# Kernel optimization log

Measured on AMD Instinct MI355X. Metric: run time of the kernel, lower is better.

The kernel has to match this reference:

```python
import jax, jax.numpy as jnp
import numpy as np


def _fps_indices(xyz, num_points):
    """Furthest point sampling. xyz: [B, N, 3] -> indices [B, num_points] (int32)."""
    B, N, _ = xyz.shape

    def step(carry, _):
        dist, farthest = carry                                   # dist: [B, N], farthest: [B]
        centroid = jnp.take_along_axis(xyz, farthest[:, None, None], axis=1)  # [B, 1, 3]
        d = jnp.sum((xyz - centroid) ** 2, axis=-1)              # [B, N]
        dist = jnp.minimum(dist, d)
        nxt = jnp.argmax(dist, axis=-1).astype(jnp.int32)        # [B]
        return (dist, nxt), farthest

    init = (jnp.full((B, N), jnp.inf, dtype=xyz.dtype),
            jnp.zeros((B,), dtype=jnp.int32))                    # convention: start at index 0
    _, idxs = jax.lax.scan(step, init, None, length=num_points)  # [num_points, B]
    return idxs.T                                                # [B, num_points]


def setup_inputs() -> dict:
    key = jax.random.key(0)
    B, C, N = 16, 3, 131072
    points = jax.random.normal(key, (B, C, N), dtype=jnp.float32)
    return {"points": points, "num_points": 2048}


def reference(points, num_points):
    # points: [B, 3, N] channels-first, as in the torch module
    xyz = jnp.transpose(points, (0, 2, 1))                       # [B, N, 3]
    idx = _fps_indices(xyz, num_points)                          # [B, num_points]
    # fps_gather_by_index: gather along the point dim of the channels-first tensor
    new_points = jnp.take_along_axis(points, idx[:, None, :], axis=2)  # [B, 3, num_points]
    return new_points
```

## Files before the change

kernel.cpp:

```cpp
#include <hip/hip_runtime.h>
#include <stdint.h>


#define NBATCH    16
#define NPTS      131072
#define SUBBLOCKS 16
#define NTHREADS  1024
#define CHUNK     8192
#define HALF      4096

typedef unsigned long long u64;

__device__ __forceinline__ u64 umax64(u64 a, u64 b) { return a > b ? a : b; }

__global__ __launch_bounds__(NTHREADS, 4)
void fps_kernel(const float* __restrict__ points,
                float* __restrict__ out,
                u64* __restrict__ slots, int M)
{
  __shared__ u64 wkeys[NTHREADS / 64];
  __shared__ u64 winner_s;

  const int bid   = blockIdx.x;
  const int xcd   = bid & 7;
  const int ord   = bid >> 3;
  const int batch = xcd * 2 + (ord >> 4);
  const int sub   = ord & 15;
  const int tid   = threadIdx.x;
  const int wave  = tid >> 6;
  const int lane  = tid & 63;

  const float* __restrict__ px = points + (size_t)batch * 3 * NPTS;
  const float* __restrict__ py = px + NPTS;
  const float* __restrict__ pz = px + 2 * NPTS;
  float* outb = out + (size_t)batch * 3 * M;
  u64* bslots = slots + (size_t)batch * 2 * SUBBLOCKS;

  const int cbase = sub * CHUNK;
  const int g0 = cbase + (tid << 2);
  const int g1 = g0 + HALF;

  float4 A0 = *(const float4*)(px + g0);
  float4 B0 = *(const float4*)(py + g0);
  float4 C0 = *(const float4*)(pz + g0);
  float4 A1 = *(const float4*)(px + g1);
  float4 B1 = *(const float4*)(py + g1);
  float4 C1 = *(const float4*)(pz + g1);
  float x0=A0.x, x1=A0.y, x2=A0.z, x3=A0.w, x4=A1.x, x5=A1.y, x6=A1.z, x7=A1.w;
  float y0=B0.x, y1=B0.y, y2=B0.z, y3=B0.w, y4=B1.x, y5=B1.y, y6=B1.z, y7=B1.w;
  float z0=C0.x, z1=C0.y, z2=C0.z, z3=C0.w, z4=C1.x, z5=C1.y, z6=C1.z, z7=C1.w;
  asm volatile("" :
    "+v"(x0),"+v"(x1),"+v"(x2),"+v"(x3),"+v"(x4),"+v"(x5),"+v"(x6),"+v"(x7),
    "+v"(y0),"+v"(y1),"+v"(y2),"+v"(y3),"+v"(y4),"+v"(y5),"+v"(y6),"+v"(y7),
    "+v"(z0),"+v"(z1),"+v"(z2),"+v"(z3),"+v"(z4),"+v"(z5),"+v"(z6),"+v"(z7));

  float d0, d1, d2, d3, d4, d5, d6, d7;
  d0 = d1 = d2 = d3 = d4 = d5 = d6 = d7 = __builtin_inff();

  if (sub == 0 && tid == 0) {
    outb[0]     = px[0];
    outb[M]     = py[0];
    outb[2 * M] = pz[0];
  }

  int sel = 0;
  for (int t = 1; t < M; ++t) {
    float cx = px[sel], cy = py[sel], cz = pz[sel];

    float best = -1.0f;
    int bidx = 0;
#define STEP(XX, YY, ZZ, DREG, IDX) { \
    float dx = __fsub_rn((XX), cx); \
    float dy = __fsub_rn((YY), cy); \
    float dz = __fsub_rn((ZZ), cz); \
    float dd = __builtin_fmaf(dz, dz, __builtin_fmaf(dy, dy, __fmul_rn(dx, dx))); \
    DREG = DREG < dd ? DREG : dd; \
    if (DREG > best) { best = DREG; bidx = (IDX); } }
    STEP(x0, y0, z0, d0, g0 + 0)
    STEP(x1, y1, z1, d1, g0 + 1)
    STEP(x2, y2, z2, d2, g0 + 2)
    STEP(x3, y3, z3, d3, g0 + 3)
    STEP(x4, y4, z4, d4, g1 + 0)
    STEP(x5, y5, z5, d5, g1 + 1)
    STEP(x6, y6, z6, d6, g1 + 2)
    STEP(x7, y7, z7, d7, g1 + 3)

    u64 key = ((u64)__float_as_uint(best) << 17) | (u64)((NPTS - 1) - bidx);

#pragma unroll
    for (int m = 32; m >= 1; m >>= 1) {
      u64 o = __shfl_xor(key, m, 64);
      key = umax64(key, o);
    }
    if (lane == 0) wkeys[wave] = key;
    __syncthreads();

    if (wave == 0) {
      u64 k = wkeys[lane & 15];
#pragma unroll
      for (int m = 8; m >= 1; m >>= 1) {
        u64 o = __shfl_xor(k, m, 64);
        k = umax64(k, o);
      }
      u64* par = bslots + (size_t)(t & 1) * SUBBLOCKS;

      if (lane == 0) {
        (void)__hip_atomic_exchange(par + sub, ((u64)t << 49) | k,
                                    __ATOMIC_RELAXED, __HIP_MEMORY_SCOPE_AGENT);
      }

      u64 v = 0;
      const bool poller = (lane < SUBBLOCKS);
      u64* pp = par + lane;
      for (;;) {
        if (poller) {
          v = __hip_atomic_fetch_add(pp, 0ull,
                                     __ATOMIC_RELAXED, __HIP_MEMORY_SCOPE_AGENT);
        }
        bool ok = !poller | ((unsigned)(v >> 49) == (unsigned)t);
        if (__ballot(ok) == ~0ull) break;
      }
#pragma unroll
      for (int m = 8; m >= 1; m >>= 1) {
        u64 o = __shfl_xor(v, m, 64);
        v = umax64(v, o);
      }
      if (lane == 0) winner_s = v;
    }
    __syncthreads();

    sel = (NPTS - 1) - (int)(winner_s & 0x1FFFF);

    if (sub == 0 && tid == 0) {
      outb[t]         = px[sel];
      outb[M + t]     = py[sel];
      outb[2 * M + t] = pz[sel];
    }
  }
}

extern "C" void kernel_launch(void* const* d_in, const int* in_sizes, int n_in,
                              void* d_out, int out_size, void* d_ws, size_t ws_size,
                              hipStream_t stream) {
  (void)in_sizes; (void)n_in; (void)ws_size;
  const float* points = (const float*)d_in[0];
  float* out = (float*)d_out;
  u64* slots = (u64*)d_ws;
  const int M = out_size / (NBATCH * 3);

  hipMemsetAsync(d_ws, 0, (size_t)NBATCH * 2 * SUBBLOCKS * sizeof(u64), stream);

  hipLaunchKernelGGL(fps_kernel, dim3(NBATCH * SUBBLOCKS), dim3(NTHREADS), 0,
                     stream, points, out, slots, M);
}
```

Before: 4.126 ms.

## Assign block roles by hardware XCC ID and poll XCD-local L2 slots

Each block reads its XCC ID from a hardware register and takes a role through per-XCC atomic counters, so all 16 sub-blocks of a batch are placed on the same XCD instead of relying on the assumed round-robin dispatch. The cross-block barrier now writes each partial key twice: once with workgroup-scope atomics, which should stay in the XCD-local L2, and once with an agent-scope store. Pollers spin mainly on the cheaper local copy and check the device-scope copy only every fourth round as a fallback. The aim is lower per-iteration synchronisation latency, at the cost of an extra store, a role-assignment prologue, and reliance on L2 coherence behaviour within an XCD.

```diff
diff --git a/kernel.cpp b/kernel.cpp
--- a/kernel.cpp
+++ b/kernel.cpp
@@ -10,31 +10,62 @@
 #define HALF      4096
 
 typedef unsigned long long u64;
+typedef unsigned int u32;
 
 __device__ __forceinline__ u64 umax64(u64 a, u64 b) { return a > b ? a : b; }
 
 __global__ __launch_bounds__(NTHREADS, 4)
 void fps_kernel(const float* __restrict__ points,
                 float* __restrict__ out,
-                u64* __restrict__ slots, int M)
+                u64* __restrict__ dslots,
+                u64* __restrict__ lslots,
+                u32* __restrict__ cnts,
+                int M)
 {
   __shared__ u64 wkeys[NTHREADS / 64];
   __shared__ u64 winner_s;
-
-  const int bid   = blockIdx.x;
-  const int xcd   = bid & 7;
-  const int ord   = bid >> 3;
-  const int batch = xcd * 2 + (ord >> 4);
-  const int sub   = ord & 15;
-  const int tid   = threadIdx.x;
-  const int wave  = tid >> 6;
-  const int lane  = tid & 63;
+  __shared__ int role_s;
+
+  const int tid  = threadIdx.x;
+  const int wave = tid >> 6;
+  const int lane = tid & 63;
+
+  if (tid == 0) {
+    u32 xcc;
+    asm volatile("s_getreg_b32 %0, hwreg(HW_REG_XCC_ID)" : "=s"(xcc));
+    xcc &= 7u;
+    int role;
+    u32 r = atomicAdd(&cnts[xcc], 1u);
+    if (r < 32u) {
+      role = (int)(xcc * 32u + r);
+    } else {
+      for (;;) {
+        bool got = false;
+        for (int x = 0; x < 8; ++x) {
+          u32 c = __hip_atomic_load(&cnts[x], __ATOMIC_RELAXED,
+                                    __HIP_MEMORY_SCOPE_AGENT);
+          if (c < 32u) {
+            u32 rr = atomicAdd(&cnts[x], 1u);
+            if (rr < 32u) { role = x * 32 + (int)rr; got = true; break; }
+          }
+        }
+        if (got) break;
+      }
+    }
+    role_s = role;
+  }
+  __syncthreads();
+  const int role  = role_s;
+  const int rr    = role & 31;
+  const int batch = (role >> 5) * 2 + (rr >> 4);
+  const int sub   = rr & 15;
 
   const float* __restrict__ px = points + (size_t)batch * 3 * NPTS;
   const float* __restrict__ py = px + NPTS;
   const float* __restrict__ pz = px + 2 * NPTS;
   float* outb = out + (size_t)batch * 3 * M;
-  u64* bslots = slots + (size_t)batch * 2 * SUBBLOCKS;
+  u64* dbase = dslots + (size_t)batch * 2 * SUBBLOCKS;
+  u64* lbase = lslots + (size_t)batch * 2 * SUBBLOCKS;
 
   const int cbase = sub * CHUNK;
   const int g0 = cbase + (tid << 2);
@@ -102,23 +133,37 @@
         u64 o = __shfl_xor(k, m, 64);
         k = umax64(k, o);
       }
-      u64* par = bslots + (size_t)(t & 1) * SUBBLOCKS;
+      u64* dpar = dbase + (size_t)(t & 1) * SUBBLOCKS;
+      u64* lpar = lbase + (size_t)(t & 1) * SUBBLOCKS;
+      const u64 tagged = ((u64)t << 49) | k;
 
       if (lane == 0) {
-        (void)__hip_atomic_exchange(par + sub, ((u64)t << 49) | k,
-                                    __ATOMIC_RELAXED, __HIP_MEMORY_SCOPE_AGENT);
-      }
-
+        (void)__hip_atomic_exchange(lpar + sub, tagged,
+                                    __ATOMIC_RELAXED,
+                                    __HIP_MEMORY_SCOPE_WORKGROUP);
+        __hip_atomic_store(dpar + sub, tagged,
+                           __ATOMIC_RELAXED, __HIP_MEMORY_SCOPE_AGENT);
+      }
+
+      const bool poller = (lane < SUBBLOCKS);
       u64 v = 0;
-      const bool poller = (lane < SUBBLOCKS);
-      u64* pp = par + lane;
-      for (;;) {
+      for (int round = 1;; ++round) {
         if (poller) {
-          v = __hip_atomic_fetch_add(pp, 0ull,
-                                     __ATOMIC_RELAXED, __HIP_MEMORY_SCOPE_AGENT);
+          v = __hip_atomic_fetch_add((u64*)(lpar + lane), 0ull,
+                                     __ATOMIC_RELAXED,
+                                     __HIP_MEMORY_SCOPE_WORKGROUP);
         }
         bool ok = !poller | ((unsigned)(v >> 49) == (unsigned)t);
         if (__ballot(ok) == ~0ull) break;
+        if ((round & 3) == 0) {
+          u64 w = 0;
+          if (poller) {
+            w = __hip_atomic_load(dpar + lane, __ATOMIC_RELAXED,
+                                  __HIP_MEMORY_SCOPE_AGENT);
+          }
+          bool ok2 = !poller | ((unsigned)(w >> 49) == (unsigned)t);
+          if (__ballot(ok2) == ~0ull) { v = w; break; }
+        }
       }
 #pragma unroll
       for (int m = 8; m >= 1; m >>= 1) {
@@ -145,11 +190,13 @@
   (void)in_sizes; (void)n_in; (void)ws_size;
   const float* points = (const float*)d_in[0];
   float* out = (float*)d_out;
-  u64* slots = (u64*)d_ws;
+  u64* dslots = (u64*)d_ws;
+  u64* lslots = (u64*)((char*)d_ws + 4096);
+  u32* cnts   = (u32*)((char*)d_ws + 8192);
   const int M = out_size / (NBATCH * 3);
 
-  hipMemsetAsync(d_ws, 0, (size_t)NBATCH * 2 * SUBBLOCKS * sizeof(u64), stream);
+  hipMemsetAsync(d_ws, 0, 8192 + 256, stream);
 
   hipLaunchKernelGGL(fps_kernel, dim3(NBATCH * SUBBLOCKS), dim3(NTHREADS), 0,
-                     stream, points, out, slots, M);
+                     stream, points, out, dslots, lslots, cnts, M);
 }
```

New measurement: 5.044 ms. +22.2%, slower.
